# Kernel tuning notes

Measured on AMD Instinct MI355X. Metric: run time of the kernel, lower is better.

Reference implementation:

```python
import jax, jax.numpy as jnp
import numpy as np

B, S, D = 4, 2048, 1024


def setup_inputs() -> dict:
    key = jax.random.key(0)
    ks = jax.random.split(key, 8)
    x = jax.random.normal(ks[0], (B, S, D), dtype=jnp.float32)
    # additive causal mask: 0 on/below diagonal, -1e9 above
    causal = jnp.tril(jnp.ones((S, S), dtype=bool))
    mask = jnp.where(causal, 0.0, -1e9).astype(jnp.float32)[None, :, :]  # [1,S,S]
    scale = 1.0 / np.sqrt(D)
    Wq = jax.random.normal(ks[1], (D, D), dtype=jnp.float32) * scale
    bq = jnp.zeros((D,), dtype=jnp.float32)
    Wk = jax.random.normal(ks[2], (D, D), dtype=jnp.float32) * scale
    bk = jnp.zeros((D,), dtype=jnp.float32)
    Wv = jax.random.normal(ks[3], (D, D), dtype=jnp.float32) * scale
    bv = jnp.zeros((D,), dtype=jnp.float32)
    return {"x": x, "mask": mask, "Wq": Wq, "bq": bq, "Wk": Wk, "bk": bk, "Wv": Wv, "bv": bv}


def reference(x, mask, Wq, bq, Wk, bk, Wv, bv):
    # Q/K/V projections (torch Linear: y = x @ W^T + b)
    q = jnp.einsum('bsd,ed->bse', x, Wq) + bq
    k = jnp.einsum('bsd,ed->bse', x, Wk) + bk
    v = jnp.einsum('bsd,ed->bse', x, Wv) + bv
    d = x.shape[-1]
    scores = jnp.einsum('bqd,bkd->bqk', q, k) / jnp.sqrt(jnp.float32(d))
    scores = scores + mask
    attn = jax.nn.softmax(scores, axis=-1)
    return jnp.einsum('bqk,bkd->bqd', attn, v)
```

## Files before the change

kernel.cpp:

```cpp
#include <hip/hip_runtime.h>
#include <hip/hip_bf16.h>


typedef __attribute__((ext_vector_type(8))) short short8;
typedef __attribute__((ext_vector_type(4))) float f32x4;
typedef __attribute__((ext_vector_type(4))) unsigned short ushort4v;

static __device__ __forceinline__ unsigned short f2b(float f) {
  union { __hip_bfloat16 h; unsigned short u; } cv;
  cv.h = __float2bfloat16(f);
  return cv.u;
}

#define GLOAD_LDS16(gsrc, ldst)                                              \
  __builtin_amdgcn_global_load_lds(                                          \
      (const __attribute__((address_space(1))) void*)(gsrc),                 \
      (__attribute__((address_space(3))) void*)(ldst), 16, 0, 0)

__global__ __launch_bounds__(256) void cvt4(const float* __restrict__ in,
                                            unsigned short* __restrict__ out, int n4) {
  int i = blockIdx.x * blockDim.x + threadIdx.x;
  if (i >= n4) return;
  float4 v = reinterpret_cast<const float4*>(in)[i];
  ushort4v o;
  o.x = f2b(v.x); o.y = f2b(v.y); o.z = f2b(v.z); o.w = f2b(v.w);
  reinterpret_cast<ushort4v*>(out)[i] = o;
}

__global__ __launch_bounds__(256) void prep_w(
    const float* __restrict__ Wq, const float* __restrict__ Wk, const float* __restrict__ Wv,
    const float* __restrict__ bq, const float* __restrict__ bk, const float* __restrict__ bv,
    unsigned short* __restrict__ Wb, float* __restrict__ biasb) {
  int id = blockIdx.x;
  if (id < 3072) {
    int sel = id >> 10;
    const float* src = sel == 0 ? Wq : sel == 1 ? Wk : Wv;
    int i = (id & 1023) * 256 + threadIdx.x;
    float4 v = reinterpret_cast<const float4*>(src)[i];
    ushort4v o;
    o.x = f2b(v.x); o.y = f2b(v.y); o.z = f2b(v.z); o.w = f2b(v.w);
    reinterpret_cast<ushort4v*>(Wb + (long)sel * 1048576)[i] = o;
  } else {
    int i = (id - 3072) * 256 + threadIdx.x;
    if (i < 3072) {
      int sel = i >> 10;
      const float* src = sel == 0 ? bq : sel == 1 ? bk : bv;
      biasb[i] = src[i & 1023];
    }
  }
}

template <int MODE>
__global__ __launch_bounds__(256, 4) void gemm128(
    const unsigned short* __restrict__ A, const unsigned short* __restrict__ B,
    void* __restrict__ Cout, const float* __restrict__ bias,
    unsigned short* __restrict__ VtOut, float scale,
    int lda, int ldb, int ldc, int ktiles,
    long aStride, long bStride, long cStride) {
  int bx = blockIdx.x, by = blockIdx.y, bz = blockIdx.z;
  if (MODE == 1 && bx > by) return;

  __shared__ unsigned short sA[128 * 64];
  __shared__ unsigned short sB[128 * 64];

  int tid = threadIdx.x;
  int lane = tid & 63;
  int w = tid >> 6;
  int wr = w >> 1, wc = w & 1;

  const unsigned short* Ab = A + bz * aStride + (long)by * 128 * lda;
  const unsigned short* Bb = B + bz * bStride + (long)bx * 128 * ldb;

  f32x4 acc[4][4];
#pragma unroll
  for (int m = 0; m < 4; ++m)
#pragma unroll
    for (int n = 0; n < 4; ++n) acc[m][n] = (f32x4){0.f, 0.f, 0.f, 0.f};

  for (int kt = 0; kt < ktiles; ++kt) {
    __syncthreads();
#pragma unroll
    for (int c = 0; c < 8; ++c) {
      int chunk = w * 8 + c;
      int half = chunk & 15;
      int L = half * 1024 + lane * 16;
      int row = L >> 7;
      int gs = ((L >> 4) & 7) ^ (row & 7);
      if (chunk < 16) {
        GLOAD_LDS16(Ab + (long)row * lda + kt * 64 + gs * 8, sA + half * 512);
      } else {
        GLOAD_LDS16(Bb + (long)row * ldb + kt * 64 + gs * 8, sB + half * 512);
      }
    }
    __syncthreads();

#pragma unroll
    for (int kk = 0; kk < 2; ++kk) {
      short8 af[4], bfr[4];
#pragma unroll
      for (int m = 0; m < 4; ++m) {
        int row = wr * 64 + m * 16 + (lane & 15);
        int g = kk * 4 + (lane >> 4);
        af[m] = *(const short8*)((const char*)sA + row * 128 + ((g ^ (row & 7)) << 4));
      }
#pragma unroll
      for (int n = 0; n < 4; ++n) {
        int row = wc * 64 + n * 16 + (lane & 15);
        int g = kk * 4 + (lane >> 4);
        bfr[n] = *(const short8*)((const char*)sB + row * 128 + ((g ^ (row & 7)) << 4));
      }
#pragma unroll
      for (int m = 0; m < 4; ++m)
#pragma unroll
        for (int n = 0; n < 4; ++n)
          acc[m][n] = __builtin_amdgcn_mfma_f32_16x16x32_bf16(af[m], bfr[n], acc[m][n], 0, 0, 0);
    }
  }

  int r0 = by * 128 + wr * 64 + (lane >> 4) * 4;
  int c0 = bx * 128 + wc * 64 + (lane & 15);
  if (MODE == 0) {
    if (bx < 16) {
      unsigned short* C = (unsigned short*)Cout;
#pragma unroll
      for (int m = 0; m < 4; ++m)
#pragma unroll
        for (int n = 0; n < 4; ++n) {
          int gc = c0 + n * 16;
          float bv = bias[gc];
#pragma unroll
          for (int r = 0; r < 4; ++r)
            C[(long)(r0 + m * 16 + r) * ldc + gc] = f2b(acc[m][n][r] + bv);
        }
    } else {
      long b = by >> 4;
      int s0 = (by & 15) * 128 + wr * 64 + (lane >> 4) * 4;
      int d0 = (bx - 16) * 128 + wc * 64 + (lane & 15);
      unsigned short* VT = VtOut + b * (1024L * 2048);
#pragma unroll
      for (int m = 0; m < 4; ++m)
#pragma unroll
        for (int n = 0; n < 4; ++n) {
          int d = d0 + n * 16;
          float bv = bias[2048 + d];
          ushort4v o;
          o.x = f2b(acc[m][n][0] + bv);
          o.y = f2b(acc[m][n][1] + bv);
          o.z = f2b(acc[m][n][2] + bv);
          o.w = f2b(acc[m][n][3] + bv);
          *(ushort4v*)(VT + (long)d * 2048 + s0 + m * 16) = o;
        }
    }
  } else {
    float* C = (float*)Cout + bz * cStride;
#pragma unroll
    for (int m = 0; m < 4; ++m)
#pragma unroll
      for (int n = 0; n < 4; ++n)
#pragma unroll
        for (int r = 0; r < 4; ++r)
          C[(long)(r0 + m * 16 + r) * ldc + c0 + n * 16] = acc[m][n][r] * scale;
  }
}

__global__ __launch_bounds__(512, 2) void pv_gemm(
    const unsigned short* __restrict__ P, const unsigned short* __restrict__ Vt,
    float* __restrict__ out) {
  __shared__ unsigned short sA[128 * 64];
  __shared__ unsigned short sB[128 * 64];
  int tid = threadIdx.x;
  int lane = tid & 63;
  int w = tid >> 6;
  int wr = w >> 2, wc = w & 3;
  int bx = blockIdx.x, byp = blockIdx.y, bz = blockIdx.z;
  const unsigned short* Pb = P + bz * (2048L * 4096);
  const unsigned short* Bb = Vt + bz * (1024L * 2048) + (long)bx * 128 * 2048;
  float* Ob = out + bz * (2048L * 1024);

#pragma unroll
  for (int half = 0; half < 2; ++half) {
    int strip = half == 0 ? (15 - byp) : byp;
    int nkt = (strip + 1) * 2;
    const unsigned short* Ab = Pb + (long)strip * 128 * 4096;

    f32x4 acc[4][2];
#pragma unroll
    for (int m = 0; m < 4; ++m)
#pragma unroll
      for (int n = 0; n < 2; ++n) acc[m][n] = (f32x4){0.f, 0.f, 0.f, 0.f};

    for (int kt = 0; kt < nkt; ++kt) {
      __syncthreads();
#pragma unroll
      for (int c = 0; c < 4; ++c) {
        int chunk = w * 4 + c;
        int hh = chunk & 15;
        int L = hh * 1024 + lane * 16;
        int row = L >> 7;
        int gs = ((L >> 4) & 7) ^ (row & 7);
        if (chunk < 16) {
          GLOAD_LDS16(Ab + (long)row * 4096 + kt * 64 + gs * 8, sA + hh * 512);
        } else {
          GLOAD_LDS16(Bb + (long)row * 2048 + kt * 64 + gs * 8, sB + hh * 512);
        }
      }
      __syncthreads();

#pragma unroll
      for (int kk = 0; kk < 2; ++kk) {
        short8 af[4], bf2[2];
#pragma unroll
        for (int m = 0; m < 4; ++m) {
          int row = wr * 64 + m * 16 + (lane & 15);
          int g = kk * 4 + (lane >> 4);
          af[m] = *(const short8*)((const char*)sA + row * 128 + ((g ^ (row & 7)) << 4));
        }
#pragma unroll
        for (int n = 0; n < 2; ++n) {
          int row = wc * 32 + n * 16 + (lane & 15);
          int g = kk * 4 + (lane >> 4);
          bf2[n] = *(const short8*)((const char*)sB + row * 128 + ((g ^ (row & 7)) << 4));
        }
#pragma unroll
        for (int m = 0; m < 4; ++m)
#pragma unroll
          for (int n = 0; n < 2; ++n)
            acc[m][n] = __builtin_amdgcn_mfma_f32_16x16x32_bf16(af[m], bf2[n], acc[m][n], 0, 0, 0);
      }
    }

    int r0 = strip * 128 + wr * 64 + (lane >> 4) * 4;
    int c0 = bx * 128 + wc * 32 + (lane & 15);
#pragma unroll
    for (int m = 0; m < 4; ++m)
#pragma unroll
      for (int n = 0; n < 2; ++n)
#pragma unroll
        for (int r = 0; r < 4; ++r)
          Ob[(long)(r0 + m * 16 + r) * 1024 + c0 + n * 16] = acc[m][n][r];
  }
}

__global__ __launch_bounds__(256) void softmax_causal(float* __restrict__ S) {
  int row = blockIdx.x;
  long b = row >> 11;
  int i = row & 2047;
  float* s = S + (b * 2048 + i) * 2048;
  unsigned short* p = (unsigned short*)s;
  int n = i + 1;
  int jEnd = ((i >> 7) + 1) << 7;
  int tid = threadIdx.x;
  __shared__ float red[4];

  float vals[8];
  float m = -3.0e38f;
#pragma unroll
  for (int k = 0; k < 8; ++k) {
    int j = tid + k * 256;
    vals[k] = (j < n) ? s[j] : -3.0e38f;
    m = fmaxf(m, vals[k]);
  }
#pragma unroll
  for (int off = 32; off > 0; off >>= 1) m = fmaxf(m, __shfl_xor(m, off));
  if ((tid & 63) == 0) red[tid >> 6] = m;
  __syncthreads();
  m = fmaxf(fmaxf(red[0], red[1]), fmaxf(red[2], red[3]));
  __syncthreads();

  float sum = 0.f;
#pragma unroll
  for (int k = 0; k < 8; ++k) {
    int j = tid + k * 256;
    float e = (j < n) ? __expf(vals[k] - m) : 0.f;
    vals[k] = e;
    sum += e;
  }
#pragma unroll
  for (int off = 32; off > 0; off >>= 1) sum += __shfl_xor(sum, off);
  if ((tid & 63) == 0) red[tid >> 6] = sum;
  __syncthreads();
  sum = red[0] + red[1] + red[2] + red[3];
  float inv = 1.0f / sum;

#pragma unroll
  for (int k = 0; k < 8; ++k) {
    int j = tid + k * 256;
    if (j < jEnd) p[j] = f2b(vals[k] * inv);
  }
}

extern "C" void kernel_launch(void* const* d_in, const int* in_sizes, int n_in,
                              void* d_out, int out_size, void* d_ws, size_t ws_size,
                              hipStream_t stream) {
  const float* x = (const float*)d_in[0];
  const float* Wq = (const float*)d_in[2];
  const float* bq = (const float*)d_in[3];
  const float* Wk = (const float*)d_in[4];
  const float* bk = (const float*)d_in[5];
  const float* Wv = (const float*)d_in[6];
  const float* bv = (const float*)d_in[7];
  float* out = (float*)d_out;

  char* ws = (char*)d_ws;
  const long MB = 1 << 20;
  unsigned short* xb = (unsigned short*)(ws);
  unsigned short* Wb = (unsigned short*)(ws + 16 * MB);
  float* biasb = (float*)(ws + 22 * MB);
  unsigned short* QK = (unsigned short*)(ws + 23 * MB);
  unsigned short* Vt = (unsigned short*)(ws + 55 * MB);
  float* Sbuf = (float*)(ws + 71 * MB);

  cvt4<<<8192, 256, 0, stream>>>(x, xb, 2097152);
  prep_w<<<3084, 256, 0, stream>>>(Wq, Wk, Wv, bq, bk, bv, Wb, biasb);

  gemm128<0><<<dim3(24, 64, 1), 256, 0, stream>>>(
      xb, Wb, QK, biasb, Vt, 1.0f, 1024, 1024, 2048, 16, 0, 0, 0);

  gemm128<1><<<dim3(16, 16, 4), 256, 0, stream>>>(
      QK, QK + 1024, Sbuf, nullptr, nullptr, 0.03125f, 2048, 2048, 2048, 16,
      2048L * 2048, 2048L * 2048, 2048L * 2048);

  softmax_causal<<<8192, 256, 0, stream>>>(Sbuf);

  pv_gemm<<<dim3(8, 8, 4), 512, 0, stream>>>((unsigned short*)Sbuf, Vt, out);
}
```

Baseline: 301.5 us.

## Split QKV projection epilogue, add separate V transpose, triangular-indexed scores grid

The projection GEMM now writes Q, K and V row-major into one packed QKV buffer instead of scattering V transposed from its epilogue. A separate LDS-tiled transpose kernel then builds Vt. The scores GEMM launches only the 136 lower-triangular tiles per batch, decoding tile coordinates from a linear index instead of launching a full grid and exiting early. Launch-bound occupancy hints are dropped and the GEMM is refactored into a templated body with lambda epilogues. It trades strided V stores in the GEMM for an extra kernel launch and an extra pass over V in memory.

```diff
diff --git a/kernel.cpp b/kernel.cpp
--- a/kernel.cpp
+++ b/kernel.cpp
@@ -50,34 +50,22 @@
   }
 }
 
-template <int MODE>
-__global__ __launch_bounds__(256, 4) void gemm128(
-    const unsigned short* __restrict__ A, const unsigned short* __restrict__ B,
-    void* __restrict__ Cout, const float* __restrict__ bias,
-    unsigned short* __restrict__ VtOut, float scale,
-    int lda, int ldb, int ldc, int ktiles,
-    long aStride, long bStride, long cStride) {
-  int bx = blockIdx.x, by = blockIdx.y, bz = blockIdx.z;
-  if (MODE == 1 && bx > by) return;
-
-  __shared__ unsigned short sA[128 * 64];
-  __shared__ unsigned short sB[128 * 64];
-
+template <typename EPI>
+static __device__ __forceinline__ void gemm128_body(
+    const unsigned short* __restrict__ Ab, const unsigned short* __restrict__ Bb,
+    int lda, int ldb, int nkt, unsigned short* sA, unsigned short* sB, EPI epi) {
   int tid = threadIdx.x;
   int lane = tid & 63;
   int w = tid >> 6;
   int wr = w >> 1, wc = w & 1;
 
-  const unsigned short* Ab = A + bz * aStride + (long)by * 128 * lda;
-  const unsigned short* Bb = B + bz * bStride + (long)bx * 128 * ldb;
-
   f32x4 acc[4][4];
 #pragma unroll
   for (int m = 0; m < 4; ++m)
 #pragma unroll
     for (int n = 0; n < 4; ++n) acc[m][n] = (f32x4){0.f, 0.f, 0.f, 0.f};
 
-  for (int kt = 0; kt < ktiles; ++kt) {
+  for (int kt = 0; kt < nkt; ++kt) {
     __syncthreads();
 #pragma unroll
     for (int c = 0; c < 8; ++c) {
@@ -116,54 +104,141 @@
           acc[m][n] = __builtin_amdgcn_mfma_f32_16x16x32_bf16(af[m], bfr[n], acc[m][n], 0, 0, 0);
     }
   }
-
-  int r0 = by * 128 + wr * 64 + (lane >> 4) * 4;
-  int c0 = bx * 128 + wc * 64 + (lane & 15);
-  if (MODE == 0) {
-    if (bx < 16) {
-      unsigned short* C = (unsigned short*)Cout;
-#pragma unroll
-      for (int m = 0; m < 4; ++m)
-#pragma unroll
-        for (int n = 0; n < 4; ++n) {
-          int gc = c0 + n * 16;
-          float bv = bias[gc];
-#pragma unroll
-          for (int r = 0; r < 4; ++r)
-            C[(long)(r0 + m * 16 + r) * ldc + gc] = f2b(acc[m][n][r] + bv);
-        }
-    } else {
-      long b = by >> 4;
-      int s0 = (by & 15) * 128 + wr * 64 + (lane >> 4) * 4;
-      int d0 = (bx - 16) * 128 + wc * 64 + (lane & 15);
-      unsigned short* VT = VtOut + b * (1024L * 2048);
-#pragma unroll
-      for (int m = 0; m < 4; ++m)
-#pragma unroll
-        for (int n = 0; n < 4; ++n) {
-          int d = d0 + n * 16;
-          float bv = bias[2048 + d];
-          ushort4v o;
-          o.x = f2b(acc[m][n][0] + bv);
-          o.y = f2b(acc[m][n][1] + bv);
-          o.z = f2b(acc[m][n][2] + bv);
-          o.w = f2b(acc[m][n][3] + bv);
-          *(ushort4v*)(VT + (long)d * 2048 + s0 + m * 16) = o;
-        }
-    }
-  } else {
-    float* C = (float*)Cout + bz * cStride;
-#pragma unroll
-    for (int m = 0; m < 4; ++m)
-#pragma unroll
-      for (int n = 0; n < 4; ++n)
-#pragma unroll
-        for (int r = 0; r < 4; ++r)
-          C[(long)(r0 + m * 16 + r) * ldc + c0 + n * 16] = acc[m][n][r] * scale;
-  }
-}
-
-__global__ __launch_bounds__(512, 2) void pv_gemm(
+  int rloc = wr * 64 + (lane >> 4) * 4;
+  int cloc = wc * 64 + (lane & 15);
+  epi(acc, rloc, cloc);
+}
+
+__global__ __launch_bounds__(256) void proj_gemm(
+    const unsigned short* __restrict__ A, const unsigned short* __restrict__ B,
+    unsigned short* __restrict__ C, const float* __restrict__ bias) {
+  __shared__ unsigned short sA[128 * 64];
+  __shared__ unsigned short sB[128 * 64];
+  int bx = blockIdx.x, by = blockIdx.y;
+  const unsigned short* Ab = A + (long)by * 128 * 1024;
+  const unsigned short* Bb = B + (long)bx * 128 * 1024;
+  gemm128_body(Ab, Bb, 1024, 1024, 16, sA, sB,
+               [&](f32x4 acc[4][4], int rloc, int cloc) {
+                 int r0 = by * 128 + rloc;
+                 int c0 = bx * 128 + cloc;
+#pragma unroll
+                 for (int m = 0; m < 4; ++m)
+#pragma unroll
+                   for (int n = 0; n < 4; ++n) {
+                     int gc = c0 + n * 16;
+                     float bv = bias[gc];
+#pragma unroll
+                     for (int r = 0; r < 4; ++r)
+                       C[(long)(r0 + m * 16 + r) * 3072 + gc] = f2b(acc[m][n][r] + bv);
+                   }
+               });
+}
+
+__global__ __launch_bounds__(256) void scores_gemm(
+    const unsigned short* __restrict__ QKV, float* __restrict__ S) {
+  __shared__ unsigned short sA[128 * 64];
+  __shared__ unsigned short sB[128 * 64];
+  int t = blockIdx.x;
+  int by = (int)((sqrtf(8.f * t + 1.f) - 1.f) * 0.5f);
+  while ((by + 1) * (by + 2) / 2 <= t) ++by;
+  while (by * (by + 1) / 2 > t) --by;
+  int bx = t - by * (by + 1) / 2;
+  long bz = blockIdx.z;
+  const unsigned short* Q = QKV + bz * (2048L * 3072);
+  const unsigned short* Ab = Q + (long)by * 128 * 3072;
+  const unsigned short* Bb = Q + 1024 + (long)bx * 128 * 3072;
+  float* Sb = S + bz * (2048L * 2048);
+  gemm128_body(Ab, Bb, 3072, 3072, 16, sA, sB,
+               [&](f32x4 acc[4][4], int rloc, int cloc) {
+                 int r0 = by * 128 + rloc;
+                 int c0 = bx * 128 + cloc;
+#pragma unroll
+                 for (int m = 0; m < 4; ++m)
+#pragma unroll
+                   for (int n = 0; n < 4; ++n)
+#pragma unroll
+                     for (int r = 0; r < 4; ++r)
+                       Sb[(long)(r0 + m * 16 + r) * 2048 + c0 + n * 16] =
+                           acc[m][n][r] * 0.03125f;
+               });
+}
+
+__global__ __launch_bounds__(256) void transpose64(const unsigned short* __restrict__ V,
+                                                   unsigned short* __restrict__ Vt) {
+  __shared__ unsigned short t[64][72];
+  int s0 = blockIdx.x * 64, d0 = blockIdx.y * 64;
+  long bz = blockIdx.z;
+  const unsigned short* src = V + bz * (2048L * 3072);
+  unsigned short* dst = Vt + bz * (1024L * 2048);
+  int tid = threadIdx.x;
+#pragma unroll
+  for (int pp = 0; pp < 2; ++pp) {
+    int r = pp * 32 + (tid >> 3);
+    int c = (tid & 7) * 8;
+    short8 v = *(const short8*)(src + (long)(s0 + r) * 3072 + d0 + c);
+    *(short8*)&t[r][c] = v;
+  }
+  __syncthreads();
+#pragma unroll
+  for (int pp = 0; pp < 2; ++pp) {
+    int d = pp * 32 + (tid >> 3);
+    int sc = (tid & 7) * 8;
+    short8 v;
+#pragma unroll
+    for (int k = 0; k < 8; ++k) v[k] = (short)t[sc + k][d];
+    *(short8*)(dst + (long)(d0 + d) * 2048 + s0 + sc) = v;
+  }
+}
+
+__global__ __launch_bounds__(256) void softmax_causal(float* __restrict__ S) {
+  int row = blockIdx.x;
+  long b = row >> 11;
+  int i = row & 2047;
+  float* s = S + (b * 2048 + i) * 2048;
+  unsigned short* p = (unsigned short*)s;
+  int n = i + 1;
+  int jEnd = ((i >> 7) + 1) << 7;
+  int tid = threadIdx.x;
+  __shared__ float red[4];
+
+  float vals[8];
+  float m = -3.0e38f;
+#pragma unroll
+  for (int k = 0; k < 8; ++k) {
+    int j = tid + k * 256;
+    vals[k] = (j < n) ? s[j] : -3.0e38f;
+    m = fmaxf(m, vals[k]);
+  }
+#pragma unroll
+  for (int off = 32; off > 0; off >>= 1) m = fmaxf(m, __shfl_xor(m, off));
+  if ((tid & 63) == 0) red[tid >> 6] = m;
+  __syncthreads();
+  m = fmaxf(fmaxf(red[0], red[1]), fmaxf(red[2], red[3]));
+  __syncthreads();
+
+  float sum = 0.f;
+#pragma unroll
+  for (int k = 0; k < 8; ++k) {
+    int j = tid + k * 256;
+    float e = (j < n) ? __expf(vals[k] - m) : 0.f;
+    vals[k] = e;
+    sum += e;
+  }
+#pragma unroll
+  for (int off = 32; off > 0; off >>= 1) sum += __shfl_xor(sum, off);
+  if ((tid & 63) == 0) red[tid >> 6] = sum;
+  __syncthreads();
+  sum = red[0] + red[1] + red[2] + red[3];
+  float inv = 1.0f / sum;
+
+#pragma unroll
+  for (int k = 0; k < 8; ++k) {
+    int j = tid + k * 256;
+    if (j < jEnd) p[j] = f2b(vals[k] * inv);
+  }
+}
+
+__global__ __launch_bounds__(512) void pv_gemm(
     const unsigned short* __restrict__ P, const unsigned short* __restrict__ Vt,
     float* __restrict__ out) {
   __shared__ unsigned short sA[128 * 64];
@@ -241,54 +316,6 @@
   }
 }
 
-__global__ __launch_bounds__(256) void softmax_causal(float* __restrict__ S) {
-  int row = blockIdx.x;
-  long b = row >> 11;
-  int i = row & 2047;
-  float* s = S + (b * 2048 + i) * 2048;
-  unsigned short* p = (unsigned short*)s;
-  int n = i + 1;
-  int jEnd = ((i >> 7) + 1) << 7;
-  int tid = threadIdx.x;
-  __shared__ float red[4];
-
-  float vals[8];
-  float m = -3.0e38f;
-#pragma unroll
-  for (int k = 0; k < 8; ++k) {
-    int j = tid + k * 256;
-    vals[k] = (j < n) ? s[j] : -3.0e38f;
-    m = fmaxf(m, vals[k]);
-  }
-#pragma unroll
-  for (int off = 32; off > 0; off >>= 1) m = fmaxf(m, __shfl_xor(m, off));
-  if ((tid & 63) == 0) red[tid >> 6] = m;
-  __syncthreads();
-  m = fmaxf(fmaxf(red[0], red[1]), fmaxf(red[2], red[3]));
-  __syncthreads();
-
-  float sum = 0.f;
-#pragma unroll
-  for (int k = 0; k < 8; ++k) {
-    int j = tid + k * 256;
-    float e = (j < n) ? __expf(vals[k] - m) : 0.f;
-    vals[k] = e;
-    sum += e;
-  }
-#pragma unroll
-  for (int off = 32; off > 0; off >>= 1) sum += __shfl_xor(sum, off);
-  if ((tid & 63) == 0) red[tid >> 6] = sum;
-  __syncthreads();
-  sum = red[0] + red[1] + red[2] + red[3];
-  float inv = 1.0f / sum;
-
-#pragma unroll
-  for (int k = 0; k < 8; ++k) {
-    int j = tid + k * 256;
-    if (j < jEnd) p[j] = f2b(vals[k] * inv);
-  }
-}
-
 extern "C" void kernel_launch(void* const* d_in, const int* in_sizes, int n_in,
                               void* d_out, int out_size, void* d_ws, size_t ws_size,
                               hipStream_t stream) {
@@ -306,19 +333,18 @@
   unsigned short* xb = (unsigned short*)(ws);
   unsigned short* Wb = (unsigned short*)(ws + 16 * MB);
   float* biasb = (float*)(ws + 22 * MB);
-  unsigned short* QK = (unsigned short*)(ws + 23 * MB);
-  unsigned short* Vt = (unsigned short*)(ws + 55 * MB);
-  float* Sbuf = (float*)(ws + 71 * MB);
+  unsigned short* QKV = (unsigned short*)(ws + 23 * MB);
+  unsigned short* Vt = (unsigned short*)(ws + 71 * MB);
+  float* Sbuf = (float*)(ws + 87 * MB);
 
   cvt4<<<8192, 256, 0, stream>>>(x, xb, 2097152);
   prep_w<<<3084, 256, 0, stream>>>(Wq, Wk, Wv, bq, bk, bv, Wb, biasb);
 
-  gemm128<0><<<dim3(24, 64, 1), 256, 0, stream>>>(
-      xb, Wb, QK, biasb, Vt, 1.0f, 1024, 1024, 2048, 16, 0, 0, 0);
-
-  gemm128<1><<<dim3(16, 16, 4), 256, 0, stream>>>(
-      QK, QK + 1024, Sbuf, nullptr, nullptr, 0.03125f, 2048, 2048, 2048, 16,
-      2048L * 2048, 2048L * 2048, 2048L * 2048);
+  proj_gemm<<<dim3(24, 64), 256, 0, stream>>>(xb, Wb, QKV, biasb);
+
+  transpose64<<<dim3(32, 16, 4), 256, 0, stream>>>(QKV + 2048, Vt);
+
+  scores_gemm<<<dim3(136, 1, 4), 256, 0, stream>>>(QKV, Sbuf);
 
   softmax_causal<<<8192, 256, 0, stream>>>(Sbuf);
 
```

Result: faster. 285.3 us (-5.4%).
